# Kernel optimization log

Hardware: AMD Instinct MI355X
Metric: run time of the kernel (lower is better)

The kernel has to match this reference:

```python
import math
import jax, jax.numpy as jnp
import numpy as np

B, L, Q, H = 4, 256, 128, 1024
TYPES = 32
LABELS = TYPES + 1
FACTOR = math.sqrt(H)


def _init(key, shape, fan_in):
    return jax.random.normal(key, shape, jnp.float32) / math.sqrt(fan_in)


def _gelu(x):
    # torch nn.GELU default = exact erf form
    return jax.nn.gelu(x, approximate=False)


def setup_inputs() -> dict:
    key = jax.random.key(0)
    ks = jax.random.split(key, 12)
    lengths = jax.random.randint(ks[0], (B,), L // 2, L + 1)
    batch_masks = jnp.arange(L)[None, :] < lengths[:, None]  # [B,L] bool
    return {
        "batch_hiddens": jax.random.normal(ks[1], (B, L, H), jnp.float32),
        "batch_masks": batch_masks,
        "queries": jax.random.normal(ks[2], (B, Q, H), jnp.float32),
        "queries_locs": jax.random.uniform(ks[3], (B, Q, 2), jnp.float32) * L,
        "queries_logits": jax.random.normal(ks[4], (B, Q, LABELS), jnp.float32),
        "cls_w1": _init(ks[5], (H, H // 2), H),
        "cls_b1": jnp.zeros((H // 2,), jnp.float32),
        "cls_w2": _init(ks[6], (H // 2, LABELS), H // 2),
        "cls_b2": jnp.zeros((LABELS,), jnp.float32),
        "tq_w": _init(ks[7], (H, 2 * H), H),
        "tq_b": jnp.zeros((2 * H,), jnp.float32),
        "tc_w": _init(ks[8], (H, 2 * H), H),
        "tc_b": jnp.zeros((2 * H,), jnp.float32),
        "loc_w1": _init(ks[9], (H, H // 2), H),
        "loc_b1": jnp.zeros((H // 2,), jnp.float32),
        "loc_w2": _init(ks[10], (H // 2, 6), H // 2) * 0.1,
        "loc_b2": jnp.zeros((6,), jnp.float32),
    }


def reference(batch_hiddens, batch_masks, queries, queries_locs, queries_logits,
              cls_w1, cls_b1, cls_w2, cls_b2, tq_w, tq_b, tc_w, tc_b,
              loc_w1, loc_b1, loc_w2, loc_b2):
    # Classifier: label probabilities fused with prior logits
    cls_logits = _gelu(queries @ cls_w1 + cls_b1) @ cls_w2 + cls_b2  # [B,Q,LABELS]
    labels_pros = jax.nn.softmax(queries_logits + cls_logits, axis=-1)

    # Bilinear start/end channel scores
    qh = (queries @ tq_w + tq_b).reshape(B, Q, 2, H)        # [B,Q,2,H]
    ch = (batch_hiddens @ tc_w + tc_b).reshape(B, L, 2, H)  # [B,L,2,H]
    score = jnp.einsum('bqch,bvch->bcqv', qh, ch) / FACTOR  # [B,2,Q,L]
    score = jnp.where(batch_masks[:, None, None, :], score, -1e8)

    # Span-pair table: all (start i <= end j); P = L*(L+1)/2
    i_idx, j_idx = jnp.triu_indices(L)
    score_p = score[:, 0][:, :, i_idx] + score[:, 1][:, :, j_idx]  # [B,Q,P]
    mask_p = batch_masks[:, j_idx]                                  # [B,P]

    # Locator: per-query Gaussian-like quadratic-form span weight
    loc_out = _gelu(queries @ loc_w1 + loc_b1) @ loc_w2 + loc_b2  # [B,Q,6]
    offsets = loc_out[..., :2]
    fac = loc_out[..., 2:].reshape(B, Q, 2, 2)
    fac = fac @ jnp.swapaxes(fac, -1, -2)  # PSD factor matrix [B,Q,2,2]
    centers = queries_locs + offsets        # [B,Q,2]
    pairs_f = jnp.stack([i_idx, j_idx], axis=-1).astype(jnp.float32)  # [P,2]
    delta = pairs_f[None, None] - centers[:, :, None, :]              # [B,Q,P,2]
    quad = jnp.einsum('bqpi,bqij,bqpj->bqp', delta, fac, delta)       # >= 0
    weight = jnp.exp(-quad) * mask_p[:, None, :].astype(score_p.dtype)

    # Weighted (fused) softmax over span pairs
    m = jnp.max(score_p, axis=-1, keepdims=True)
    e = weight * jnp.exp(score_p - m)
    locs_pros = e / (jnp.sum(e, axis=-1, keepdims=True) + 1e-12)
    return labels_pros, locs_pros
```

## Files before the change

### kernel.cpp

```cpp
#include <hip/hip_runtime.h>
#include <math.h>

typedef _Float16 f16;
typedef __attribute__((ext_vector_type(4))) _Float16 f16x4;
typedef __attribute__((ext_vector_type(8))) _Float16 f16x8;
typedef __attribute__((ext_vector_type(4))) float f32x4;

#define Bn 4
#define Ln 256
#define Qn 128
#define Hn 1024
#define LBL 33
#define POUT 32896

__device__ __forceinline__ float gelu_exact(float x){
    return 0.5f * x * (1.0f + erff(x * 0.70710678118654752f));
}

__device__ __forceinline__ bool mask_at(const void* m, int idx, unsigned u0){
    if (u0 == 0x01010101u) return ((const unsigned char*)m)[idx] != 0;
    if (u0 == 0x3f800000u) return ((const float*)m)[idx] != 0.0f;
    return ((const int*)m)[idx] != 0;
}

__device__ __forceinline__ void gload16(const void* g, void* l){
    __builtin_amdgcn_global_load_lds(
        (const __attribute__((address_space(1))) unsigned int*)g,
        (__attribute__((address_space(3))) unsigned int*)l, 16, 0, 0);
}

__global__ __launch_bounds__(256) void prep(
    const float* __restrict__ q, const float* __restrict__ h,
    const float* __restrict__ cls_w1, const float* __restrict__ loc_w1,
    const float* __restrict__ tq_w,  const float* __restrict__ tc_w,
    f16* __restrict__ qf, f16* __restrict__ hf,
    f16* __restrict__ Wq_t, f16* __restrict__ Wc_t)
{
    const int bx = blockIdx.x, t = threadIdx.x;
    if (bx < 1536) {
        if (bx < 512) {
            const int gid = bx*256 + t;
            const float4 v = ((const float4*)q)[gid];
            f16x4 o; o[0]=(f16)v.x; o[1]=(f16)v.y; o[2]=(f16)v.z; o[3]=(f16)v.w;
            *(f16x4*)&qf[(size_t)gid*4] = o;
        } else {
            const int gid = (bx-512)*256 + t;
            const float4 v = ((const float4*)h)[gid];
            f16x4 o; o[0]=(f16)v.x; o[1]=(f16)v.y; o[2]=(f16)v.z; o[3]=(f16)v.w;
            *(f16x4*)&hf[(size_t)gid*4] = o;
        }
        return;
    }
    const int tile = bx - 1536;
    const float* src; f16* dst; int id, lg;
    if      (tile < 256)  { id = tile;        src = cls_w1; dst = Wq_t;                     lg = 4; }
    else if (tile < 512)  { id = tile - 256;  src = loc_w1; dst = Wq_t + (size_t)512*1024;  lg = 4; }
    else if (tile < 1536) { id = tile - 512;  src = tq_w;   dst = Wq_t + (size_t)1024*1024; lg = 6; }
    else                  { id = tile - 1536; src = tc_w;   dst = Wc_t;                     lg = 6; }
    const int N  = 32 << lg;
    const int n0 = (id & ((1<<lg)-1)) * 32;
    const int k0 = (id >> lg) * 64;

    __shared__ float X[64][33];
    const int rr = t >> 3, c4 = (t & 7) * 4;
    const float4 v0 = *(const float4*)&src[(size_t)(k0 + rr)      * N + n0 + c4];
    const float4 v1 = *(const float4*)&src[(size_t)(k0 + rr + 32) * N + n0 + c4];
    X[rr   ][c4+0] = v0.x; X[rr   ][c4+1] = v0.y; X[rr   ][c4+2] = v0.z; X[rr   ][c4+3] = v0.w;
    X[rr+32][c4+0] = v1.x; X[rr+32][c4+1] = v1.y; X[rr+32][c4+2] = v1.z; X[rr+32][c4+3] = v1.w;
    __syncthreads();
    const int n = t >> 3, kc = (t & 7) * 8;
    f16x8 o;
    #pragma unroll
    for (int u = 0; u < 8; u++) o[u] = (f16)X[kc + u][n];
    *(f16x8*)&dst[(size_t)(n0 + n) * 1024 + k0 + kc] = o;
}

__global__ __launch_bounds__(256) void gemm128(
    const f16* __restrict__ Aq, const f16* __restrict__ Ac,
    const f16* __restrict__ Wq, const f16* __restrict__ Wc,
    const float* __restrict__ cb1, const float* __restrict__ lb1,
    const float* __restrict__ tqb, const float* __restrict__ tcb,
    float* __restrict__ X1, float* __restrict__ X2,
    f16* __restrict__ qh, f16* __restrict__ chh)
{
    __shared__ __align__(16) f16 Ah[128*64];
    __shared__ __align__(16) f16 Bh[64*64];
    const int tid = threadIdx.x;
    const int w = tid >> 6, lane = tid & 63;
    const int wr = w >> 1, wcc = w & 1;
    const int lr = lane & 15, hi = lane >> 4;

    const int bx = blockIdx.x;
    const f16 *A, *Bt;
    int bm, bn, qside;
    if (bx < 192) { qside = 1; bm = bx / 48; bn = bx % 48; A = Aq; Bt = Wq; }
    else          { qside = 0; const int ix = bx - 192; bm = ix >> 5; bn = ix & 31; A = Ac; Bt = Wc; }

    const int lr8   = lane >> 3;
    const int lslot = (lane & 7) ^ lr8;
    const f16* Ag = A  + (size_t)(bm*128 + w*32) * 1024;
    const f16* Bg = Bt + (size_t)(bn*64 + w*16) * 1024;
    f16* AhW = &Ah[(w*32)*64];
    f16* BhW = &Bh[(w*16)*64];

    f32x4 acc[4][2] = {};

    for (int k0 = 0; k0 < 1024; k0 += 64) {
        #pragma unroll
        for (int i = 0; i < 4; i++)
            gload16(Ag + (size_t)(i*8 + lr8)*1024 + k0 + lslot*8, AhW + i*8*64);
        #pragma unroll
        for (int i = 0; i < 2; i++)
            gload16(Bg + (size_t)(i*8 + lr8)*1024 + k0 + lslot*8, BhW + i*8*64);
        __syncthreads();
        #pragma unroll
        for (int ks = 0; ks < 2; ks++) {
            f16x8 a[4], b[2];
            #pragma unroll
            for (int mf = 0; mf < 4; mf++) {
                const int row = wr*64 + mf*16 + lr;
                const int sl  = (ks*4 + hi) ^ (lr & 7);
                a[mf] = *(const f16x8*)&Ah[row*64 + sl*8];
            }
            #pragma unroll
            for (int nf = 0; nf < 2; nf++) {
                const int row = wcc*32 + nf*16 + lr;
                const int sl  = (ks*4 + hi) ^ (lr & 7);
                b[nf] = *(const f16x8*)&Bh[row*64 + sl*8];
            }
            #pragma unroll
            for (int mf = 0; mf < 4; mf++)
                #pragma unroll
                for (int nf = 0; nf < 2; nf++)
                    acc[mf][nf] = __builtin_amdgcn_mfma_f32_16x16x32_f16(a[mf], b[nf], acc[mf][nf], 0, 0, 0);
        }
        __syncthreads();
    }

    const int r0 = hi * 4;
    #pragma unroll
    for (int nf = 0; nf < 2; nf++) {
        const int colg = bn*64 + wcc*32 + nf*16 + lr;
        if (qside) {
            if (bn < 8) {
                const float bv = cb1[colg];
                #pragma unroll
                for (int mf = 0; mf < 4; mf++)
                    #pragma unroll
                    for (int r = 0; r < 4; r++) {
                        const int row = bm*128 + wr*64 + mf*16 + r0 + r;
                        X1[(size_t)row*512 + colg] = gelu_exact(acc[mf][nf][r] + bv);
                    }
            } else if (bn < 16) {
                const int c2 = colg - 512;
                const float bv = lb1[c2];
                #pragma unroll
                for (int mf = 0; mf < 4; mf++)
                    #pragma unroll
                    for (int r = 0; r < 4; r++) {
                        const int row = bm*128 + wr*64 + mf*16 + r0 + r;
                        X2[(size_t)row*512 + c2] = gelu_exact(acc[mf][nf][r] + bv);
                    }
            } else {
                const int c2 = colg - 1024;
                const float bv = tqb[c2];
                #pragma unroll
                for (int mf = 0; mf < 4; mf++)
                    #pragma unroll
                    for (int r = 0; r < 4; r++) {
                        const int row = bm*128 + wr*64 + mf*16 + r0 + r;
                        qh[(size_t)row*2048 + c2] = (f16)(acc[mf][nf][r] + bv);
                    }
            }
        } else {
            const float bv = tcb[colg];
            #pragma unroll
            for (int mf = 0; mf < 4; mf++)
                #pragma unroll
                for (int r = 0; r < 4; r++) {
                    const int row = bm*128 + wr*64 + mf*16 + r0 + r;
                    chh[(size_t)row*2048 + colg] = (f16)(acc[mf][nf][r] + bv);
                }
        }
    }
}

__global__ __launch_bounds__(256) void score_heads(
    const f16* __restrict__ qh, const f16* __restrict__ chh,
    const void* __restrict__ maskp, float* __restrict__ score,
    const float* __restrict__ X1, const float* __restrict__ cls_w2,
    const float* __restrict__ cls_b2, const float* __restrict__ qlog, float* __restrict__ out0,
    const float* __restrict__ X2, const float* __restrict__ loc_w2,
    const float* __restrict__ loc_b2, const float* __restrict__ qlocs, float* __restrict__ geo)
{
    __shared__ __align__(16) char smem[64*72*2*2 + 64];
    const int bx = blockIdx.x, tid = threadIdx.x;

    if (bx < 128) {
        f16* Ah = (f16*)smem;
        f16* Bh = Ah + 32*72;
        const int bc = bx & 7, b = bc >> 1, c = bc & 1;
        const int n0 = ((bx >> 3) & 3) * 64;
        const int m0 = (bx >> 5) * 32;
        const f16* Aq = qh  + (size_t)b*Qn*2048 + c*1024;
        const f16* Bv = chh + (size_t)b*Ln*2048 + c*1024;

        const int w = tid >> 6, lane = tid & 63;
        const int wr = w >> 1, wc = w & 1;
        const int lr = lane & 15, lk = (lane >> 4) * 8;
        const int rr = tid >> 3, gg = (tid & 7) * 8;

        f32x4 acc[2] = {};

        for (int k0 = 0; k0 < 1024; k0 += 64) {
            *(f16x8*)&Ah[(rr   )*72 + gg] = *(const f16x8*)(Aq + (size_t)(m0+rr   )*2048 + k0 + gg);
            *(f16x8*)&Bh[(rr   )*72 + gg] = *(const f16x8*)(Bv + (size_t)(n0+rr   )*2048 + k0 + gg);
            *(f16x8*)&Bh[(rr+32)*72 + gg] = *(const f16x8*)(Bv + (size_t)(n0+rr+32)*2048 + k0 + gg);
            __syncthreads();
            #pragma unroll
            for (int ks=0; ks<64; ks+=32){
                f16x8 a, b2[2];
                a = *(f16x8*)&Ah[(wr*16+lr)*72 + ks+lk];
                #pragma unroll
                for (int nf=0; nf<2; nf++) b2[nf] = *(f16x8*)&Bh[(wc*32+nf*16+lr)*72 + ks+lk];
                #pragma unroll
                for (int nf=0; nf<2; nf++)
                    acc[nf] = __builtin_amdgcn_mfma_f32_16x16x32_f16(a, b2[nf], acc[nf], 0, 0, 0);
            }
            __syncthreads();
        }

        const unsigned u0 = *(const unsigned*)maskp;
        const int r0 = (lane >> 4) * 4;
        #pragma unroll
        for (int nf=0; nf<2; nf++){
            const int v = n0 + wc*32 + nf*16 + lr;
            const bool mv = mask_at(maskp, b*Ln + v, u0);
            #pragma unroll
            for (int r=0; r<4; r++){
                const int q = m0 + wr*16 + r0 + r;
                float val = mv ? (acc[nf][r] * 0.03125f) : -100000000.0f;
                score[((size_t)(b*2+c)*Qn + q)*Ln + v] = val;
            }
        }
    } else if (bx < 640) {
        float* xr = (float*)smem;
        float* lg = xr + 512;
        float* sc = lg + 64;
        const int row = bx - 128, t = tid;
        xr[t]       = X1[(size_t)row*512 + t];
        xr[t + 256] = X1[(size_t)row*512 + t + 256];
        __syncthreads();
        const int c = t >> 2, s = t & 3;
        float acc = 0.0f;
        if (c < LBL){
            for (int k = s*128; k < (s+1)*128; k++) acc += xr[k] * cls_w2[(size_t)k*LBL + c];
        }
        acc += __shfl_down(acc, 1);
        acc += __shfl_down(acc, 2);
        if (s == 0 && c < LBL) lg[c] = acc + cls_b2[c] + qlog[(size_t)row*LBL + c];
        __syncthreads();
        if (t == 0){
            float mx = -1e30f;
            for (int k=0;k<LBL;k++) mx = fmaxf(mx, lg[k]);
            float sm = 0.0f;
            for (int k=0;k<LBL;k++) sm += __expf(lg[k]-mx);
            sc[0] = mx; sc[1] = 1.0f / sm;
        }
        __syncthreads();
        if (t < LBL) out0[(size_t)row*LBL + t] = __expf(lg[t]-sc[0]) * sc[1];
    } else {
        float* xr = (float*)smem;
        float* lg = xr + 512;
        const int row = bx - 640, t = tid;
        xr[t]       = X2[(size_t)row*512 + t];
        xr[t + 256] = X2[(size_t)row*512 + t + 256];
        __syncthreads();
        const int c = t >> 5, s = t & 31;
        float acc = 0.0f;
        if (c < 6){
            for (int k = s*16; k < (s+1)*16; k++) acc += xr[k] * loc_w2[(size_t)k*6 + c];
        }
        #pragma unroll
        for (int off=1; off<32; off<<=1) acc += __shfl_down(acc, off);
        if (s == 0 && c < 6) lg[c] = acc + loc_b2[c];
        __syncthreads();
        if (t == 0){
            const float o0=lg[0], o1=lg[1], f0=lg[2], f1=lg[3], f2=lg[4], f3=lg[5];
            geo[(size_t)row*5+0] = qlocs[(size_t)row*2+0] + o0;
            geo[(size_t)row*5+1] = qlocs[(size_t)row*2+1] + o1;
            geo[(size_t)row*5+2] = f0*f0 + f1*f1;
            geo[(size_t)row*5+3] = f0*f2 + f1*f3;
            geo[(size_t)row*5+4] = f2*f2 + f3*f3;
        }
    }
}

__global__ __launch_bounds__(1024, 8) void pair_fused(
    const float* __restrict__ score, const float* __restrict__ geo,
    float* __restrict__ out1)
{
    const int bq = blockIdx.x, b = bq >> 7, t = threadIdx.x;
    __shared__ float s0[256], s1[256];
    __shared__ float2 RG[256];
    __shared__ float T[288];
    __shared__ float red[16];
    __shared__ float bcv;

    const float* sc0 = score + ((size_t)(b*2)*Qn + (bq & 127))*Ln;
    if (t < 256)      s0[t]       = sc0[t];
    else if (t < 512) s1[t - 256] = sc0[(size_t)Qn*Ln + (t - 256)];
    __syncthreads();

    const int lane = t & 63;
    const float4 s1v = *(const float4*)&s1[lane*4];
    const float4 s0v = *(const float4*)&s0[lane*4];
    float sfx = fmaxf(fmaxf(s1v.x, s1v.y), fmaxf(s1v.z, s1v.w));
    #pragma unroll
    for (int off = 1; off < 64; off <<= 1) {
        const int src = (lane + off < 64) ? (lane + off) : 63;
        const float v = __shfl(sfx, src, 64);
        if (lane + off < 64) sfx = fmaxf(sfx, v);
    }
    float nxt = __shfl(sfx, (lane < 63) ? (lane + 1) : 63, 64);
    if (lane == 63) nxt = -3.0e38f;
    float run = fmaxf(nxt, s1v.w);
    float cand = s0v.w + run;
    run = fmaxf(run, s1v.z); cand = fmaxf(cand, s0v.z + run);
    run = fmaxf(run, s1v.y); cand = fmaxf(cand, s0v.y + run);
    run = fmaxf(run, s1v.x); cand = fmaxf(cand, s0v.x + run);
    #pragma unroll
    for (int off = 1; off < 64; off <<= 1) cand = fmaxf(cand, __shfl_xor(cand, off, 64));
    const float m = cand;

    const float c0  = geo[(size_t)bq*5+0], c1  = geo[(size_t)bq*5+1];
    const float F00 = geo[(size_t)bq*5+2], F01 = geo[(size_t)bq*5+3], F11 = geo[(size_t)bq*5+4];

    if (t < 256) {
        const float d0 = (float)t - c0;
        const float nG = -2.0f * F01 * d0;
        const float Rv = s0[t] - F00 * d0 * d0 - m;
        RG[t] = make_float2(Rv - nG * c1, nG);
        const float d1 = (float)t - c1;
        T[t + (t >> 3)] = s1[t] - F11 * d1 * d1;
    }
    __syncthreads();

    float ev[32];
    float lsum = 0.0f;
    #pragma unroll
    for (int kk = 0; kk < 8; kk++) {
        const int p = kk*4096 + 4*t;
        const float sq = sqrtf((float)(263169 - 8*p));
        int i = (int)((513.0f - sq) * 0.5f);
        int j = i + (p - ((i*(513 - i)) >> 1));
        #pragma unroll
        for (int u = 0; u < 4; u++) {
            const float2 rg = RG[i];
            const float e = __expf(fmaf(rg.y, (float)j, rg.x) + T[j + (j >> 3)]);
            ev[kk*4 + u] = e;
            lsum += e;
            j++;
            const bool wrap = (j > 255);
            i += wrap ? 1 : 0;
            j = wrap ? i : j;
        }
    }
    if (t < 32) {
        const int p = 32768 + 4*t;
        const float sq = sqrtf((float)(263169 - 8*p));
        int i = (int)((513.0f - sq) * 0.5f);
        int j = i + (p - ((i*(513 - i)) >> 1));
        #pragma unroll
        for (int u = 0; u < 4; u++) {
            const float2 rg = RG[i];
            lsum += __expf(fmaf(rg.y, (float)j, rg.x) + T[j + (j >> 3)]);
            j++;
            const bool wrap = (j > 255);
            i += wrap ? 1 : 0;
            j = wrap ? i : j;
        }
    }

    #pragma unroll
    for (int off = 1; off < 64; off <<= 1) lsum += __shfl_xor(lsum, off, 64);
    if (lane == 0) red[t >> 6] = lsum;
    __syncthreads();
    if (t == 0) {
        float tot = 0.0f;
        #pragma unroll
        for (int k = 0; k < 16; k++) tot += red[k];
        bcv = 1.0f / (tot + 1e-12f);
    }
    __syncthreads();
    const float inv = bcv;

    float* op = out1 + (size_t)bq * POUT;
    #pragma unroll
    for (int kk = 0; kk < 8; kk++) {
        const int p = kk*4096 + 4*t;
        f32x4 v;
        v[0] = ev[kk*4]*inv; v[1] = ev[kk*4+1]*inv; v[2] = ev[kk*4+2]*inv; v[3] = ev[kk*4+3]*inv;
        *(f32x4*)&op[p] = v;
    }
    if (t < 32) {
        const int p = 32768 + 4*t;
        const float sq = sqrtf((float)(263169 - 8*p));
        int i = (int)((513.0f - sq) * 0.5f);
        int j = i + (p - ((i*(513 - i)) >> 1));
        f32x4 v;
        #pragma unroll
        for (int u = 0; u < 4; u++) {
            const float2 rg = RG[i];
            v[u] = __expf(fmaf(rg.y, (float)j, rg.x) + T[j + (j >> 3)]) * inv;
            j++;
            const bool wrap = (j > 255);
            i += wrap ? 1 : 0;
            j = wrap ? i : j;
        }
        *(f32x4*)&op[p] = v;
    }
}

extern "C" void kernel_launch(void* const* d_in, const int* in_sizes, int n_in,
                              void* d_out, int out_size, void* d_ws, size_t ws_size,
                              hipStream_t stream)
{
    const float* hiddens = (const float*)d_in[0];
    const void*  masks   = d_in[1];
    const float* queries = (const float*)d_in[2];
    const float* qlocs   = (const float*)d_in[3];
    const float* qlogits = (const float*)d_in[4];
    const float* cls_w1  = (const float*)d_in[5];
    const float* cls_b1  = (const float*)d_in[6];
    const float* cls_w2  = (const float*)d_in[7];
    const float* cls_b2  = (const float*)d_in[8];
    const float* tq_w    = (const float*)d_in[9];
    const float* tq_b    = (const float*)d_in[10];
    const float* tc_w    = (const float*)d_in[11];
    const float* tc_b    = (const float*)d_in[12];
    const float* loc_w1  = (const float*)d_in[13];
    const float* loc_b1  = (const float*)d_in[14];
    const float* loc_w2  = (const float*)d_in[15];
    const float* loc_b2  = (const float*)d_in[16];

    char* ws = (char*)d_ws;
    f16*   qf16  = (f16*)  (ws);
    f16*   hf16  = (f16*)  (ws + (1u<<20));
    float* X1    = (float*)(ws + (3u<<20));
    float* X2    = (float*)(ws + (4u<<20));
    f16*   qh    = (f16*)  (ws + (5u<<20));
    float* score = (float*)(ws + (7u<<20));
    float* geo   = (float*)(ws + (8u<<20));

    float* out0 = (float*)d_out;
    float* out1 = out0 + (size_t)Bn*Qn*LBL;

    f16* Wq_t = (f16*)out1;
    f16* Wc_t = (f16*)((char*)out1 + 6291456);
    f16* chh  = (f16*)((char*)out1 + 6291456 + 4194304);

    prep<<<dim3(4096), 256, 0, stream>>>(queries, hiddens, cls_w1, loc_w1, tq_w, tc_w,
                                         qf16, hf16, Wq_t, Wc_t);
    gemm128<<<dim3(448), 256, 0, stream>>>(qf16, hf16, Wq_t, Wc_t,
                                           cls_b1, loc_b1, tq_b, tc_b,
                                           X1, X2, qh, chh);
    score_heads<<<dim3(1152), 256, 0, stream>>>(qh, chh, masks, score,
                                                X1, cls_w2, cls_b2, qlogits, out0,
                                                X2, loc_w2, loc_b2, qlocs, geo);
    pair_fused<<<dim3(Bn*Qn), 1024, 0, stream>>>(score, geo, out1);
}
```

Measured before the change: 64.77 us.

## Split fused pair softmax into sum pass and recompute-store pass

The single pair kernel, which kept 32 exp values per thread in registers between the reduction and the store, is split in two. The first kernel computes only the max and the normalising sum and writes them per query. The second kernel uses 4x more 256-thread blocks to recompute the exponentials and write normalised outputs. This cuts register pressure and raises parallelism for the store phase, at the cost of computing every exp twice and adding one kernel launch.

```diff
diff --git a/kernel.cpp b/kernel.cpp
--- a/kernel.cpp
+++ b/kernel.cpp
@@ -296,16 +296,15 @@
     }
 }
 
-__global__ __launch_bounds__(1024, 8) void pair_fused(
+__global__ __launch_bounds__(1024, 8) void pair_sum(
     const float* __restrict__ score, const float* __restrict__ geo,
-    float* __restrict__ out1)
+    float2* __restrict__ minv)
 {
     const int bq = blockIdx.x, b = bq >> 7, t = threadIdx.x;
     __shared__ float s0[256], s1[256];
     __shared__ float2 RG[256];
     __shared__ float T[288];
     __shared__ float red[16];
-    __shared__ float bcv;
 
     const float* sc0 = score + ((size_t)(b*2)*Qn + (bq & 127))*Ln;
     if (t < 256)      s0[t]       = sc0[t];
@@ -346,28 +345,10 @@
     }
     __syncthreads();
 
-    float ev[32];
     float lsum = 0.0f;
     #pragma unroll
     for (int kk = 0; kk < 8; kk++) {
         const int p = kk*4096 + 4*t;
-        const float sq = sqrtf((float)(263169 - 8*p));
-        int i = (int)((513.0f - sq) * 0.5f);
-        int j = i + (p - ((i*(513 - i)) >> 1));
-        #pragma unroll
-        for (int u = 0; u < 4; u++) {
-            const float2 rg = RG[i];
-            const float e = __expf(fmaf(rg.y, (float)j, rg.x) + T[j + (j >> 3)]);
-            ev[kk*4 + u] = e;
-            lsum += e;
-            j++;
-            const bool wrap = (j > 255);
-            i += wrap ? 1 : 0;
-            j = wrap ? i : j;
-        }
-    }
-    if (t < 32) {
-        const int p = 32768 + 4*t;
         const float sq = sqrtf((float)(263169 - 8*p));
         int i = (int)((513.0f - sq) * 0.5f);
         int j = i + (p - ((i*(513 - i)) >> 1));
@@ -381,6 +362,21 @@
             j = wrap ? i : j;
         }
     }
+    if (t < 32) {
+        const int p = 32768 + 4*t;
+        const float sq = sqrtf((float)(263169 - 8*p));
+        int i = (int)((513.0f - sq) * 0.5f);
+        int j = i + (p - ((i*(513 - i)) >> 1));
+        #pragma unroll
+        for (int u = 0; u < 4; u++) {
+            const float2 rg = RG[i];
+            lsum += __expf(fmaf(rg.y, (float)j, rg.x) + T[j + (j >> 3)]);
+            j++;
+            const bool wrap = (j > 255);
+            i += wrap ? 1 : 0;
+            j = wrap ? i : j;
+        }
+    }
 
     #pragma unroll
     for (int off = 1; off < 64; off <<= 1) lsum += __shfl_xor(lsum, off, 64);
@@ -390,21 +386,60 @@
         float tot = 0.0f;
         #pragma unroll
         for (int k = 0; k < 16; k++) tot += red[k];
-        bcv = 1.0f / (tot + 1e-12f);
+        minv[bq] = make_float2(m, 1.0f / (tot + 1e-12f));
+    }
+}
+
+__global__ __launch_bounds__(256) void pair_store(
+    const float* __restrict__ score, const float* __restrict__ geo,
+    const float2* __restrict__ minv, float* __restrict__ out1)
+{
+    const int bx = blockIdx.x, t = threadIdx.x;
+    const int bq = bx >> 2, qtr = bx & 3;
+    const int b = bq >> 7;
+    __shared__ float2 RG[256];
+    __shared__ float T[288];
+
+    const float2 mi = minv[bq];
+    const float m = mi.x, inv = mi.y;
+    const float c0  = geo[(size_t)bq*5+0], c1  = geo[(size_t)bq*5+1];
+    const float F00 = geo[(size_t)bq*5+2], F01 = geo[(size_t)bq*5+3], F11 = geo[(size_t)bq*5+4];
+
+    const float* sc0 = score + ((size_t)(b*2)*Qn + (bq & 127))*Ln;
+    {
+        const float s0v = sc0[t];
+        const float s1v = sc0[(size_t)Qn*Ln + t];
+        const float d0 = (float)t - c0;
+        const float nG = -2.0f * F01 * d0;
+        const float Rv = s0v - F00 * d0 * d0 - m;
+        RG[t] = make_float2(Rv - nG * c1, nG);
+        const float d1 = (float)t - c1;
+        T[t + (t >> 3)] = s1v - F11 * d1 * d1;
     }
     __syncthreads();
-    const float inv = bcv;
 
     float* op = out1 + (size_t)bq * POUT;
+    const int base = qtr * 8224;
     #pragma unroll
     for (int kk = 0; kk < 8; kk++) {
-        const int p = kk*4096 + 4*t;
+        const int p = base + kk*1024 + 4*t;
+        const float sq = sqrtf((float)(263169 - 8*p));
+        int i = (int)((513.0f - sq) * 0.5f);
+        int j = i + (p - ((i*(513 - i)) >> 1));
         f32x4 v;
-        v[0] = ev[kk*4]*inv; v[1] = ev[kk*4+1]*inv; v[2] = ev[kk*4+2]*inv; v[3] = ev[kk*4+3]*inv;
+        #pragma unroll
+        for (int u = 0; u < 4; u++) {
+            const float2 rg = RG[i];
+            v[u] = __expf(fmaf(rg.y, (float)j, rg.x) + T[j + (j >> 3)]) * inv;
+            j++;
+            const bool wrap = (j > 255);
+            i += wrap ? 1 : 0;
+            j = wrap ? i : j;
+        }
         *(f32x4*)&op[p] = v;
     }
-    if (t < 32) {
-        const int p = 32768 + 4*t;
+    if (t < 8) {
+        const int p = base + 8192 + 4*t;
         const float sq = sqrtf((float)(263169 - 8*p));
         int i = (int)((513.0f - sq) * 0.5f);
         int j = i + (p - ((i*(513 - i)) >> 1));
@@ -445,13 +480,14 @@
     const float* loc_b2  = (const float*)d_in[16];
 
     char* ws = (char*)d_ws;
-    f16*   qf16  = (f16*)  (ws);
-    f16*   hf16  = (f16*)  (ws + (1u<<20));
-    float* X1    = (float*)(ws + (3u<<20));
-    float* X2    = (float*)(ws + (4u<<20));
-    f16*   qh    = (f16*)  (ws + (5u<<20));
-    float* score = (float*)(ws + (7u<<20));
-    float* geo   = (float*)(ws + (8u<<20));
+    f16*    qf16  = (f16*)   (ws);
+    f16*    hf16  = (f16*)   (ws + (1u<<20));
+    float*  X1    = (float*) (ws + (3u<<20));
+    float*  X2    = (float*) (ws + (4u<<20));
+    f16*    qh    = (f16*)   (ws + (5u<<20));
+    float*  score = (float*) (ws + (7u<<20));
+    float*  geo   = (float*) (ws + (8u<<20));
+    float2* minv  = (float2*)(ws + (8u<<20) + 0x8000);
 
     float* out0 = (float*)d_out;
     float* out1 = out0 + (size_t)Bn*Qn*LBL;
@@ -468,5 +504,6 @@
     score_heads<<<dim3(1152), 256, 0, stream>>>(qh, chh, masks, score,
                                                 X1, cls_w2, cls_b2, qlogits, out0,
                                                 X2, loc_w2, loc_b2, qlocs, geo);
-    pair_fused<<<dim3(Bn*Qn), 1024, 0, stream>>>(score, geo, out1);
-}
+    pair_sum  <<<dim3(Bn*Qn), 1024, 0, stream>>>(score, geo, minv);
+    pair_store<<<dim3(Bn*Qn*4), 256, 0, stream>>>(score, geo, minv, out1);
+}
```

Measured after the change: 70.34 us. 8.6% more time.
